# Kernel tuning notes

Measured on AMD Instinct MI355X. Metric: run time of the kernel, lower is better.

## Reference

```python
import jax, jax.numpy as jnp
import numpy as np

OBS = 256      # observation_space_size == state_vector_len
SV = 2047      # STATE_VECTORS = WMG_MAX_OBS
D = 256        # tfm_vec_size = 8 heads * 32 head_size
H = 8
HD = 32
L = 2          # TFM_NUM_LAYERS
FF = 1024      # TFM_HIDDEN_SIZE
ACH = 512      # AC_HIDDEN_LAYER_SIZE
A = 16         # action_space_size


def setup_inputs() -> dict:
    key = jax.random.key(0)
    ks = jax.random.split(key, 24)
    r = lambda k, s: (jax.random.normal(k, s, jnp.float32) * 0.02)
    inp = {
        "observation": jax.random.normal(ks[0], (OBS,), jnp.float32),
        "old_vectors": jax.random.normal(ks[1], (SV, OBS), jnp.float32),
        "W_core": r(ks[2], (OBS, D)), "b_core": jnp.zeros((D,), jnp.float32),
        # memo embedding takes cat(state_vec, age_onehot) of size OBS+SV
        "W_memo": r(ks[3], (OBS + SV, D)), "b_memo": jnp.zeros((D,), jnp.float32),
        "Wq": r(ks[4], (L, D, D)), "bq": jnp.zeros((L, D), jnp.float32),
        "Wk": r(ks[5], (L, D, D)), "bk": jnp.zeros((L, D), jnp.float32),
        "Wv": r(ks[6], (L, D, D)), "bv": jnp.zeros((L, D), jnp.float32),
        "Wo": r(ks[7], (L, D, D)), "bo": jnp.zeros((L, D), jnp.float32),
        "ln1_g": jnp.ones((L, D), jnp.float32), "ln1_b": jnp.zeros((L, D), jnp.float32),
        "ln2_g": jnp.ones((L, D), jnp.float32), "ln2_b": jnp.zeros((L, D), jnp.float32),
        "W_ff1": r(ks[8], (L, D, FF)), "b_ff1": jnp.zeros((L, FF), jnp.float32),
        "W_ff2": r(ks[9], (L, FF, D)), "b_ff2": jnp.zeros((L, D), jnp.float32),
        "aW1": r(ks[10], (D, ACH)), "ab1": jnp.zeros((ACH,), jnp.float32),
        "aW2": r(ks[11], (ACH, ACH)), "ab2": jnp.zeros((ACH,), jnp.float32),
        "aWo": r(ks[12], (ACH, A)), "abo": jnp.zeros((A,), jnp.float32),
        "cW1": r(ks[13], (D, ACH)), "cb1": jnp.zeros((ACH,), jnp.float32),
        "cW2": r(ks[14], (ACH, ACH)), "cb2": jnp.zeros((ACH,), jnp.float32),
        "cWo": r(ks[15], (ACH, 1)), "cbo": jnp.zeros((1,), jnp.float32),
    }
    return inp


def _ln(x, g, b, eps=1e-5):
    m = jnp.mean(x, axis=-1, keepdims=True)
    v = jnp.mean(jnp.square(x - m), axis=-1, keepdims=True)
    return (x - m) * jax.lax.rsqrt(v + eps) * g + b


def reference(observation, old_vectors, W_core, b_core, W_memo, b_memo,
              Wq, bq, Wk, bk, Wv, bv, Wo, bo,
              ln1_g, ln1_b, ln2_g, ln2_b, W_ff1, b_ff1, W_ff2, b_ff2,
              aW1, ab1, aW2, ab2, aWo, abo, cW1, cb1, cW2, cb2, cWo, cbo):
    # core embedding [D]
    emb0 = observation @ W_core + b_core
    # fused memo + age-onehot embedding: cat(vec_i, e_i) @ W_memo == vec_i @ W_memo[:OBS] + W_memo[OBS+i]
    memo_emb = old_vectors @ W_memo[:OBS] + W_memo[OBS:] + b_memo  # [SV, D]
    x = jnp.concatenate([emb0[None, :], memo_emb], axis=0)[None]   # [1, 1+SV, D]
    S = 1 + SV
    scale = 1.0 / np.sqrt(HD).astype(np.float32)
    for l in range(L):
        q = (x @ Wq[l] + bq[l]).reshape(1, S, H, HD)
        k = (x @ Wk[l] + bk[l]).reshape(1, S, H, HD)
        v = (x @ Wv[l] + bv[l]).reshape(1, S, H, HD)
        scores = jnp.einsum('bqhd,bkhd->bhqk', q, k) * scale       # [1,H,S,S]
        probs = jax.nn.softmax(scores, axis=-1)
        ctx = jnp.einsum('bhqk,bkhd->bqhd', probs, v).reshape(1, S, D)
        x = _ln(x + ctx @ Wo[l] + bo[l], ln1_g[l], ln1_b[l])
        h = jax.nn.gelu(x @ W_ff1[l] + b_ff1[l])
        x = _ln(x + h @ W_ff2[l] + b_ff2[l], ln2_g[l], ln2_b[l])
    t = x[:, 0, :]                                                 # [1, D]
    ha = jnp.tanh(jnp.tanh(t @ aW1 + ab1) @ aW2 + ab2)
    policy = ha @ aWo + abo                                        # [1, A] logits
    hc = jnp.tanh(jnp.tanh(t @ cW1 + cb1) @ cW2 + cb2)
    value_est = hc @ cWo + cbo                                     # [1, 1]
    # WMG_MAX_MEMOS == 0 path: new state vector is tanh(observation)
    new_vector = jnp.tanh(observation)                             # [OBS]
    return value_est, policy, new_vector
```

## Files before the change

### kernel.cpp

```cpp
#include <hip/hip_runtime.h>
#include <stdint.h>

typedef __attribute__((ext_vector_type(8))) short bf16x8;
typedef __attribute__((ext_vector_type(4))) float f32x4;

constexpr int kSEQ = 2048;
constexpr int kD   = 256;
constexpr int kHD  = 32;
constexpr int kFF  = 1024;
constexpr int kA   = 16;

__device__ __forceinline__ unsigned short f2b(float f) {
  union { float f; unsigned int u; } v; v.f = f;
  unsigned int r = v.u + 0x7FFFu + ((v.u >> 16) & 1u);
  return (unsigned short)(r >> 16);
}

struct ConvTable {
  const float* src[13];
  int K[13];
  int N[13];
  int dst[13];
  int tstart[14];
};

union SharedU {
  struct { unsigned short lt[64][72]; } cv;
  struct { unsigned short Al[64][40]; unsigned short Bl[32][40]; } g64;
  struct { unsigned short Kl[64][40]; unsigned short Vt[32][72];
           unsigned short Pl[4][16][72]; } at;
  struct { unsigned short As[16][264]; float2 red[4][16]; } lg;
};

struct MegaParams {
  ConvTable tab;
  const float *obs, *oldv, *Wcore, *bcore, *Wmemo0, *bmemo, *Wmemo2;
  const float *bq, *bk, *bv, *bo, *ln1g, *ln1b, *ln2g, *ln2b, *bff1, *bff2;
  const float *aW1, *ab1, *aW2, *ab2, *aWo, *abo;
  const float *cW1, *cb1, *cW2, *cb2, *cWo, *cbo;
  float* xf; unsigned short* xb;
  unsigned short *qb, *kb, *vb, *hb, *wT;
  float *pacc, *pml, *pf, *out;
  int oQKV[2], oWoT[2], oFF1[2], oFF2[2];
  int convJobs, nsplit, tpb;
};

__device__ void conv_job(const MegaParams& p, SharedU& sh, int job) {
  const int tid = threadIdx.x;
  if (job == p.convJobs) {
    float a = p.bcore[tid];
    #pragma unroll 8
    for (int k = 0; k < 256; k++) a += p.obs[k] * p.Wcore[k * kD + tid];
    p.xf[tid] = a;
    p.xb[tid] = f2b(a);
    return;
  }
  int m = 0;
  while (job >= p.tab.tstart[m + 1]) m++;
  const int tloc = job - p.tab.tstart[m];
  const int N = p.tab.N[m], K = p.tab.K[m];
  const int ntile = N >> 6;
  const int k0 = (tloc / ntile) * 64, n0 = (tloc % ntile) * 64;
  const float* src = p.tab.src[m];
  {
    const int r = tid >> 2, c16 = (tid & 3) * 16;
    const float* sp = src + (size_t)(k0 + r) * N + n0 + c16;
    #pragma unroll
    for (int j = 0; j < 16; j++) sh.cv.lt[r][c16 + j] = f2b(sp[j]);
  }
  __syncthreads();
  {
    const int n = tid >> 2, kc = (tid & 3) * 16;
    unsigned short* dp = p.wT + p.tab.dst[m] + (size_t)(n0 + n) * K + k0 + kc;
    unsigned short g[16];
    #pragma unroll
    for (int j = 0; j < 16; j++) g[j] = sh.cv.lt[kc + j][n];
    *(bf16x8*)dp = *(bf16x8*)&g[0];
    *(bf16x8*)(dp + 8) = *(bf16x8*)&g[8];
  }
}

__device__ void memo_job(const MegaParams& p, SharedU& sh, int job) {
  const int tid = threadIdx.x;
  const int w = tid >> 6, l = tid & 63, lg = l >> 4, lr = l & 15;
  const int sr = tid >> 2, sk = (tid & 3) * 8;
  const int kr = tid >> 3, nc = (tid & 7) * 4;
  const int m0 = (job & 31) * 64, n0 = (job >> 5) * 32;
  f32x4 acc[2];
  #pragma unroll
  for (int c = 0; c < 2; c++)
    #pragma unroll
    for (int i = 0; i < 4; i++) acc[c][i] = 0.f;

  auto loadA = [&](int k0) -> bf16x8 {
    bf16x8 av;
    if (m0 + sr < 2047) {
      const float* ap = p.oldv + (size_t)(m0 + sr) * 256 + k0 + sk;
      #pragma unroll
      for (int j = 0; j < 8; j++) av[j] = (short)f2b(ap[j]);
    } else {
      #pragma unroll
      for (int j = 0; j < 8; j++) av[j] = 0;
    }
    return av;
  };
  auto loadB = [&](int k0, float* b4) {
    const float* bp = p.Wmemo0 + (size_t)(k0 + kr) * kD + n0 + nc;
    #pragma unroll
    for (int j = 0; j < 4; j++) b4[j] = bp[j];
  };

  bf16x8 av = loadA(0);
  float b4[4];
  loadB(0, b4);

  for (int k0 = 0; k0 < 256; k0 += 32) {
    __syncthreads();
    *(bf16x8*)&sh.g64.Al[sr][sk] = av;
    #pragma unroll
    for (int j = 0; j < 4; j++) sh.g64.Bl[nc + j][kr] = f2b(b4[j]);
    __syncthreads();
    if (k0 + 32 < 256) {
      av = loadA(k0 + 32);
      loadB(k0 + 32, b4);
    }
    bf16x8 af = *(bf16x8*)&sh.g64.Al[w * 16 + lr][8 * lg];
    #pragma unroll
    for (int c = 0; c < 2; c++) {
      bf16x8 bf = *(bf16x8*)&sh.g64.Bl[c * 16 + lr][8 * lg];
      acc[c] = __builtin_amdgcn_mfma_f32_16x16x32_bf16(af, bf, acc[c], 0, 0, 0);
    }
  }

  #pragma unroll
  for (int c = 0; c < 2; c++)
    #pragma unroll
    for (int i = 0; i < 4; i++) {
      const int gr = m0 + w * 16 + 4 * lg + i;
      const int gc = n0 + c * 16 + lr;
      if (gr >= 2047) continue;
      const float v = acc[c][i] + p.bmemo[gc] + p.Wmemo2[(size_t)gr * kD + gc];
      p.xf[(size_t)(gr + 1) * kD + gc] = v;
      p.xb[(size_t)(gr + 1) * kD + gc] = f2b(v);
    }
}

__global__ __launch_bounds__(256) void k_cvm(MegaParams p) {
  __shared__ SharedU sh;
  if (blockIdx.x < 256) memo_job(p, sh, blockIdx.x);
  else conv_job(p, sh, blockIdx.x - 256);
}

template <int EPI>
__device__ __forceinline__ void gemm_job(
    SharedU& sh, int m0, int n0, const unsigned short* Ap, int lda, int Kloop,
    const unsigned short* BT, int ldb,
    const float* p0, const float* p1, const float* p2,
    void* o0, void* o1, void* o2) {
  const int tid = threadIdx.x;
  const int w = tid >> 6, l = tid & 63, lg = l >> 4, lr = l & 15;
  const int sr = tid >> 2, sk = (tid & 3) * 8;
  f32x4 acc[2];
  #pragma unroll
  for (int c = 0; c < 2; c++)
    #pragma unroll
    for (int i = 0; i < 4; i++) acc[c][i] = 0.f;

  bf16x8 av = *(const bf16x8*)(Ap + (size_t)(m0 + sr) * lda + sk);
  bf16x8 bv;
  if (tid < 128) bv = *(const bf16x8*)(BT + (size_t)(n0 + sr) * ldb + sk);

  for (int k0 = 0; k0 < Kloop; k0 += 32) {
    __syncthreads();
    *(bf16x8*)&sh.g64.Al[sr][sk] = av;
    if (tid < 128) *(bf16x8*)&sh.g64.Bl[sr][sk] = bv;
    __syncthreads();
    if (k0 + 32 < Kloop) {
      av = *(const bf16x8*)(Ap + (size_t)(m0 + sr) * lda + k0 + 32 + sk);
      if (tid < 128)
        bv = *(const bf16x8*)(BT + (size_t)(n0 + sr) * ldb + k0 + 32 + sk);
    }
    bf16x8 af = *(bf16x8*)&sh.g64.Al[w * 16 + lr][8 * lg];
    #pragma unroll
    for (int c = 0; c < 2; c++) {
      bf16x8 bf = *(bf16x8*)&sh.g64.Bl[c * 16 + lr][8 * lg];
      acc[c] = __builtin_amdgcn_mfma_f32_16x16x32_bf16(af, bf, acc[c], 0, 0, 0);
    }
  }

  #pragma unroll
  for (int c = 0; c < 2; c++) {
    #pragma unroll
    for (int i = 0; i < 4; i++) {
      const int gr = m0 + w * 16 + 4 * lg + i;
      const int gc = n0 + c * 16 + lr;
      float v = acc[c][i];
      if constexpr (EPI == 1) {
        const int t = gc >> 8, cc = gc & 255;
        const float* bp = (t == 0) ? p0 : (t == 1 ? p1 : p2);
        unsigned short* op = (t == 0) ? (unsigned short*)o0
                              : (t == 1 ? (unsigned short*)o1
                                        : (unsigned short*)o2);
        v += bp[cc];
        if (t == 0) v *= 0.17677669529663687f;
        op[(size_t)gr * kD + cc] = f2b(v);
      } else if constexpr (EPI == 2) {
        v += p0[gc];
        const float g =
            0.5f * v *
            (1.0f + tanhf(0.7978845608028654f * (v + 0.044715f * v * v * v)));
        ((unsigned short*)o0)[(size_t)gr * kFF + gc] = f2b(g);
      } else {
        ((float*)o0)[(size_t)gr * kD + gc] = v;
      }
    }
  }
}

__global__ __launch_bounds__(256) void k_qkv(MegaParams p, int lyr) {
  __shared__ SharedU sh;
  for (int job = blockIdx.x; job < 768; job += gridDim.x) {
    const int m0 = (job & 31) * 64, n0 = (job >> 5) * 32;
    gemm_job<1>(sh, m0, n0, p.xb, 256, 256, p.wT + p.oQKV[lyr], 256,
                p.bq + lyr * 256, p.bk + lyr * 256, p.bv + lyr * 256,
                p.qb, p.kb, p.vb);
  }
}

__global__ __launch_bounds__(256) void k_ff1(MegaParams p, int lyr) {
  __shared__ SharedU sh;
  for (int job = blockIdx.x; job < 1024; job += gridDim.x) {
    const int m0 = (job & 31) * 64, n0 = (job >> 5) * 32;
    gemm_job<2>(sh, m0, n0, p.xb, 256, 256, p.wT + p.oFF1[lyr], 256,
                p.bff1 + lyr * 1024, nullptr, nullptr, p.hb, nullptr, nullptr);
  }
}

__global__ __launch_bounds__(256) void k_ff2p(MegaParams p, int lyr) {
  __shared__ SharedU sh;
  for (int job = blockIdx.x; job < 1024; job += gridDim.x) {
    const int m0 = (job & 31) * 64;
    const int n0 = ((job >> 5) & 7) * 32;
    const int kc = (job >> 8) * 256;
    gemm_job<3>(sh, m0, n0, p.hb + kc, kFF, 256,
                p.wT + p.oFF2[lyr] + kc, kFF, nullptr, nullptr, nullptr,
                p.pf + (size_t)(job >> 8) * kSEQ * kD, nullptr, nullptr);
  }
}

__device__ void attn_job(SharedU& sh, int qb_, int h, int s, int tpb,
                         const unsigned short* q, const unsigned short* k,
                         const unsigned short* v, float* pacc, float* pml) {
  const int tid = threadIdx.x;
  const int w = tid >> 6, l = tid & 63, lg = l >> 4, lr = l & 15;
  const int q0 = qb_ * 64;
  const int hoff = h * kHD;
  const int sr = tid >> 2, sk = (tid & 3) * 8;
  const int t0 = s * tpb;

  const bf16x8 qf =
      *(const bf16x8*)(q + (size_t)(q0 + w * 16 + lr) * kD + hoff + 8 * lg);

  float m_[4], l_[4];
  f32x4 acc[2];
  #pragma unroll
  for (int i = 0; i < 4; i++) { m_[i] = -1e30f; l_[i] = 0.f; }
  #pragma unroll
  for (int dt = 0; dt < 2; dt++)
    #pragma unroll
    for (int i = 0; i < 4; i++) acc[dt][i] = 0.f;

  bf16x8 kreg = *(const bf16x8*)(k + (size_t)(t0 * 64 + sr) * kD + hoff + sk);
  bf16x8 vreg = *(const bf16x8*)(v + (size_t)(t0 * 64 + sr) * kD + hoff + sk);

  for (int t = 0; t < tpb; t++) {
    __syncthreads();
    *(bf16x8*)&sh.at.Kl[sr][sk] = kreg;
    #pragma unroll
    for (int j = 0; j < 8; j++) sh.at.Vt[sk + j][sr] = (unsigned short)vreg[j];
    __syncthreads();
    if (t + 1 < tpb) {
      const size_t nx = (size_t)((t0 + t + 1) * 64 + sr) * kD + hoff + sk;
      kreg = *(const bf16x8*)(k + nx);
      vreg = *(const bf16x8*)(v + nx);
    }
    f32x4 sc[4];
    #pragma unroll
    for (int c = 0; c < 4; c++) {
      f32x4 z;
      #pragma unroll
      for (int i = 0; i < 4; i++) z[i] = 0.f;
      bf16x8 kf = *(bf16x8*)&sh.at.Kl[c * 16 + lr][8 * lg];
      sc[c] = __builtin_amdgcn_mfma_f32_16x16x32_bf16(qf, kf, z, 0, 0, 0);
    }
    float tm[4];
    #pragma unroll
    for (int i = 0; i < 4; i++)
      tm[i] = fmaxf(fmaxf(sc[0][i], sc[1][i]), fmaxf(sc[2][i], sc[3][i]));
    #pragma unroll
    for (int mm = 1; mm <= 8; mm <<= 1)
      #pragma unroll
      for (int i = 0; i < 4; i++) tm[i] = fmaxf(tm[i], __shfl_xor(tm[i], mm));
    float pv[4][4], rs[4], corr[4];
    #pragma unroll
    for (int i = 0; i < 4; i++) {
      const float nm = fmaxf(m_[i], tm[i]);
      corr[i] = __expf(m_[i] - nm);
      m_[i] = nm;
      rs[i] = 0.f;
    }
    #pragma unroll
    for (int c = 0; c < 4; c++)
      #pragma unroll
      for (int i = 0; i < 4; i++) {
        pv[c][i] = __expf(sc[c][i] - m_[i]);
        rs[i] += pv[c][i];
      }
    #pragma unroll
    for (int mm = 1; mm <= 8; mm <<= 1)
      #pragma unroll
      for (int i = 0; i < 4; i++) rs[i] += __shfl_xor(rs[i], mm);
    #pragma unroll
    for (int i = 0; i < 4; i++) {
      l_[i] = l_[i] * corr[i] + rs[i];
      acc[0][i] *= corr[i];
      acc[1][i] *= corr[i];
    }
    #pragma unroll
    for (int c = 0; c < 4; c++)
      #pragma unroll
      for (int i = 0; i < 4; i++)
        sh.at.Pl[w][4 * lg + i][c * 16 + lr] = f2b(pv[c][i]);
    __syncthreads();
    #pragma unroll
    for (int k2 = 0; k2 < 2; k2++) {
      bf16x8 pf_ = *(bf16x8*)&sh.at.Pl[w][lr][k2 * 32 + 8 * lg];
      #pragma unroll
      for (int dt = 0; dt < 2; dt++) {
        bf16x8 vf = *(bf16x8*)&sh.at.Vt[dt * 16 + lr][k2 * 32 + 8 * lg];
        acc[dt] = __builtin_amdgcn_mfma_f32_16x16x32_bf16(pf_, vf, acc[dt], 0, 0, 0);
      }
    }
  }

  const int pb = s * 8 + h;
  float* pa = pacc + (size_t)pb * kSEQ * kHD;
  float* pm = pml + (size_t)pb * kSEQ * 2;
  #pragma unroll
  for (int dt = 0; dt < 2; dt++)
    #pragma unroll
    for (int i = 0; i < 4; i++) {
      const int gr = q0 + w * 16 + 4 * lg + i;
      pa[(size_t)gr * kHD + dt * 16 + lr] = acc[dt][i];
    }
  if (lr == 0) {
    #pragma unroll
    for (int i = 0; i < 4; i++) {
      const int gr = q0 + w * 16 + 4 * lg + i;
      float2 ml; ml.x = m_[i]; ml.y = l_[i];
      *(float2*)&pm[(size_t)gr * 2] = ml;
    }
  }
}

__global__ __launch_bounds__(256) void k_attn(MegaParams p) {
  __shared__ SharedU sh;
  const int njobs = 256 * p.nsplit;
  for (int job = blockIdx.x; job < njobs; job += gridDim.x) {
    const int qb_ = job & 31, h = (job >> 5) & 7, s = job >> 8;
    attn_job(sh, qb_, h, s, p.tpb, p.qb, p.kb, p.vb, p.pacc, p.pml);
  }
}

__device__ __forceinline__ void ln_write(SharedU& sh, float vloc[4][4], int r0,
                                         const float* gam, const float* bet,
                                         float* xf, unsigned short* xb) {
  const int tid = threadIdx.x;
  const int w = tid >> 6, l = tid & 63, lg = l >> 4, lr = l & 15;
  float ps[4], ps2[4];
  #pragma unroll
  for (int i = 0; i < 4; i++) {
    ps[i] = 0.f; ps2[i] = 0.f;
    #pragma unroll
    for (int c = 0; c < 4; c++) {
      ps[i] += vloc[c][i];
      ps2[i] += vloc[c][i] * vloc[c][i];
    }
  }
  #pragma unroll
  for (int mm = 1; mm <= 8; mm <<= 1)
    #pragma unroll
    for (int i = 0; i < 4; i++) {
      ps[i] += __shfl_xor(ps[i], mm);
      ps2[i] += __shfl_xor(ps2[i], mm);
    }
  if (lr == 0) {
    #pragma unroll
    for (int i = 0; i < 4; i++) {
      float2 t; t.x = ps[i]; t.y = ps2[i];
      sh.lg.red[w][4 * lg + i] = t;
    }
  }
  __syncthreads();
  #pragma unroll
  for (int i = 0; i < 4; i++) {
    const int ri = 4 * lg + i;
    float sx = 0.f, sx2 = 0.f;
    #pragma unroll
    for (int ww = 0; ww < 4; ww++) {
      float2 t = sh.lg.red[ww][ri];
      sx += t.x; sx2 += t.y;
    }
    const float mean = sx * (1.0f / 256.0f);
    const float var = sx2 * (1.0f / 256.0f) - mean * mean;
    const float rstd = rsqrtf(var + 1e-5f);
    const int gr = r0 + ri;
    #pragma unroll
    for (int c = 0; c < 4; c++) {
      const int col = w * 64 + c * 16 + lr;
      const float y = (vloc[c][i] - mean) * rstd * gam[col] + bet[col];
      xf[(size_t)gr * kD + col] = y;
      xb[(size_t)gr * kD + col] = f2b(y);
    }
  }
}

__global__ __launch_bounds__(256) void k_woln(MegaParams p, int lyr) {
  __shared__ SharedU sh;
  const unsigned short* BT = p.wT + p.oWoT[lyr];
  const float* bias = p.bo + lyr * kD;
  const float* gam = p.ln1g + lyr * kD;
  const float* bet = p.ln1b + lyr * kD;
  const int tid = threadIdx.x;
  const int w = tid >> 6, l = tid & 63, lg = l >> 4, lr = l & 15;
  for (int job = blockIdx.x; job < 128; job += gridDim.x) {
    const int r0 = job * 16;
    __syncthreads();
    {
      const int row = r0 + (tid >> 4);
      const int kc = (tid & 15) * 16;
      const int h_ = kc >> 5;
      float mx = -1e30f;
      for (int s2 = 0; s2 < p.nsplit; s2++)
        mx = fmaxf(mx, p.pml[((size_t)(s2 * 8 + h_) * kSEQ + row) * 2]);
      float L = 0.f;
      const int d0 = kc & 31;
      float o[16];
      #pragma unroll
      for (int j = 0; j < 16; j++) o[j] = 0.f;
      for (int s2 = 0; s2 < p.nsplit; s2++) {
        const size_t pb = (size_t)(s2 * 8 + h_) * kSEQ + row;
        const float2 t = *(const float2*)&p.pml[pb * 2];
        const float es = __expf(t.x - mx);
        L += t.y * es;
        const float* pa = p.pacc + pb * kHD + d0;
        #pragma unroll
        for (int j = 0; j < 16; j++) o[j] += pa[j] * es;
      }
      const float inv = 1.0f / L;
      unsigned short* dst = &sh.lg.As[tid >> 4][kc];
      #pragma unroll
      for (int j = 0; j < 16; j++) dst[j] = f2b(o[j] * inv);
    }
    __syncthreads();
    f32x4 acc[4];
    #pragma unroll
    for (int c = 0; c < 4; c++)
      #pragma unroll
      for (int i = 0; i < 4; i++) acc[c][i] = 0.f;
    #pragma unroll 2
    for (int k0 = 0; k0 < 256; k0 += 32) {
      bf16x8 af = *(bf16x8*)&sh.lg.As[lr][k0 + 8 * lg];
      #pragma unroll
      for (int c = 0; c < 4; c++) {
        bf16x8 bf = *(const bf16x8*)(BT + (size_t)(w * 64 + c * 16 + lr) * 256 +
                                     k0 + 8 * lg);
        acc[c] = __builtin_amdgcn_mfma_f32_16x16x32_bf16(af, bf, acc[c], 0, 0, 0);
      }
    }
    float vloc[4][4];
    #pragma unroll
    for (int c = 0; c < 4; c++)
      #pragma unroll
      for (int i = 0; i < 4; i++) {
        const int col = w * 64 + c * 16 + lr;
        const int gr = r0 + 4 * lg + i;
        vloc[c][i] = acc[c][i] + bias[col] + p.xf[(size_t)gr * kD + col];
      }
    ln_write(sh, vloc, r0, gam, bet, p.xf, p.xb);
  }
}

template <bool WH>
__global__ __launch_bounds__(256) void k_ln2r(MegaParams p, int lyr) {
  __shared__ float tl[256];
  __shared__ float hA[1024];
  __shared__ float hB[1024];
  __shared__ float vred[4];
  const float* bias = p.bff2 + lyr * kD;
  const float* gam = p.ln2g + lyr * kD;
  const float* bet = p.ln2b + lyr * kD;
  const int tid = threadIdx.x;
  const int w = tid >> 6, l = tid & 63;
  const int row = blockIdx.x * 4 + w;
  f32x4 v = *(const f32x4*)(p.xf + (size_t)row * kD + l * 4);
  f32x4 b4 = *(const f32x4*)(bias + l * 4);
  #pragma unroll
  for (int i = 0; i < 4; i++) v[i] += b4[i];
  #pragma unroll
  for (int s = 0; s < 4; s++) {
    f32x4 t = *(const f32x4*)(p.pf + ((size_t)s * kSEQ + row) * kD + l * 4);
    #pragma unroll
    for (int i = 0; i < 4; i++) v[i] += t[i];
  }
  float su = v[0] + v[1] + v[2] + v[3];
  #pragma unroll
  for (int mm = 1; mm < 64; mm <<= 1) su += __shfl_xor(su, mm);
  const float mn = su * (1.0f / 256.0f);
  const float d0 = v[0] - mn, d1 = v[1] - mn, d2 = v[2] - mn, d3 = v[3] - mn;
  float s2 = d0 * d0 + d1 * d1 + d2 * d2 + d3 * d3;
  #pragma unroll
  for (int mm = 1; mm < 64; mm <<= 1) s2 += __shfl_xor(s2, mm);
  const float rstd = rsqrtf(s2 * (1.0f / 256.0f) + 1e-5f);
  f32x4 g4 = *(const f32x4*)(gam + l * 4);
  f32x4 be4 = *(const f32x4*)(bet + l * 4);
  f32x4 y;
  y[0] = d0 * rstd * g4[0] + be4[0];
  y[1] = d1 * rstd * g4[1] + be4[1];
  y[2] = d2 * rstd * g4[2] + be4[2];
  y[3] = d3 * rstd * g4[3] + be4[3];
  *(f32x4*)(p.xf + (size_t)row * kD + l * 4) = y;
  unsigned long long pk = (unsigned long long)f2b(y[0]) |
                          ((unsigned long long)f2b(y[1]) << 16) |
                          ((unsigned long long)f2b(y[2]) << 32) |
                          ((unsigned long long)f2b(y[3]) << 48);
  *(unsigned long long*)(p.xb + (size_t)row * kD + l * 4) = pk;

  if constexpr (WH) {
    if (blockIdx.x == 0) {
      if (w == 0) *(f32x4*)&tl[l * 4] = y;
      __syncthreads();
      float a0 = p.ab1[tid], a1 = p.ab1[tid + 256];
      float c0 = p.cb1[tid], c1 = p.cb1[tid + 256];
      for (int k = 0; k < 256; k++) {
        const float x = tl[k];
        a0 += x * p.aW1[(size_t)k * 512 + tid];
        a1 += x * p.aW1[(size_t)k * 512 + tid + 256];
        c0 += x * p.cW1[(size_t)k * 512 + tid];
        c1 += x * p.cW1[(size_t)k * 512 + tid + 256];
      }
      hA[tid] = tanhf(a0); hA[tid + 256] = tanhf(a1);
      hA[512 + tid] = tanhf(c0); hA[768 + tid] = tanhf(c1);
      __syncthreads();
      float b0 = p.ab2[tid], b1 = p.ab2[tid + 256];
      float e0 = p.cb2[tid], e1 = p.cb2[tid + 256];
      for (int k = 0; k < 512; k++) {
        const float xa = hA[k], xc = hA[512 + k];
        b0 += xa * p.aW2[(size_t)k * 512 + tid];
        b1 += xa * p.aW2[(size_t)k * 512 + tid + 256];
        e0 += xc * p.cW2[(size_t)k * 512 + tid];
        e1 += xc * p.cW2[(size_t)k * 512 + tid + 256];
      }
      hB[tid] = tanhf(b0); hB[tid + 256] = tanhf(b1);
      hB[512 + tid] = tanhf(e0); hB[768 + tid] = tanhf(e1);
      __syncthreads();
      const int g = tid >> 4, l16 = tid & 15;
      float s = 0.f;
      for (int k2 = l16 * 32; k2 < l16 * 32 + 32; k2++)
        s += hB[k2] * p.aWo[(size_t)k2 * kA + g];
      #pragma unroll
      for (int mm = 1; mm <= 8; mm <<= 1) s += __shfl_xor(s, mm);
      if (l16 == 0) p.out[1 + g] = s + p.abo[g];
      float vv = hB[512 + tid] * p.cWo[tid] + hB[768 + tid] * p.cWo[tid + 256];
      #pragma unroll
      for (int mm = 1; mm <= 32; mm <<= 1) vv += __shfl_xor(vv, mm);
      if ((tid & 63) == 0) vred[tid >> 6] = vv;
      __syncthreads();
      if (tid == 0)
        p.out[0] = vred[0] + vred[1] + vred[2] + vred[3] + p.cbo[0];
      p.out[17 + tid] = tanhf(p.obs[tid]);
    }
  }
}

extern "C" void kernel_launch(void* const* d_in, const int* in_sizes, int n_in,
                              void* d_out, int out_size, void* d_ws, size_t ws_size,
                              hipStream_t stream) {
  const float* obs   = (const float*)d_in[0];
  const float* oldv  = (const float*)d_in[1];
  const float* Wcore = (const float*)d_in[2];
  const float* bcore = (const float*)d_in[3];
  const float* Wmemo = (const float*)d_in[4];
  const float* bmemo = (const float*)d_in[5];
  const float* Wq    = (const float*)d_in[6];
  const float* bq    = (const float*)d_in[7];
  const float* Wk    = (const float*)d_in[8];
  const float* bk    = (const float*)d_in[9];
  const float* Wv    = (const float*)d_in[10];
  const float* bv    = (const float*)d_in[11];
  const float* Wo    = (const float*)d_in[12];
  const float* bo    = (const float*)d_in[13];
  const float* ln1g  = (const float*)d_in[14];
  const float* ln1b  = (const float*)d_in[15];
  const float* ln2g  = (const float*)d_in[16];
  const float* ln2b  = (const float*)d_in[17];
  const float* Wff1  = (const float*)d_in[18];
  const float* bff1  = (const float*)d_in[19];
  const float* Wff2  = (const float*)d_in[20];
  const float* bff2  = (const float*)d_in[21];

  MegaParams P;
  P.obs = obs; P.oldv = oldv; P.Wcore = Wcore; P.bcore = bcore;
  P.Wmemo0 = Wmemo; P.bmemo = bmemo; P.Wmemo2 = Wmemo + 256 * 256;
  P.bq = bq; P.bk = bk; P.bv = bv; P.bo = bo;
  P.ln1g = ln1g; P.ln1b = ln1b; P.ln2g = ln2g; P.ln2b = ln2b;
  P.bff1 = bff1; P.bff2 = bff2;
  P.aW1 = (const float*)d_in[22]; P.ab1 = (const float*)d_in[23];
  P.aW2 = (const float*)d_in[24]; P.ab2 = (const float*)d_in[25];
  P.aWo = (const float*)d_in[26]; P.abo = (const float*)d_in[27];
  P.cW1 = (const float*)d_in[28]; P.cb1 = (const float*)d_in[29];
  P.cW2 = (const float*)d_in[30]; P.cb2 = (const float*)d_in[31];
  P.cWo = (const float*)d_in[32]; P.cbo = (const float*)d_in[33];

  char* ws = (char*)d_ws;
  P.xf = (float*)(ws + 0);
  P.xb = (unsigned short*)(ws + (2u << 20));
  P.qb = (unsigned short*)(ws + (3u << 20));
  P.kb = (unsigned short*)(ws + (4u << 20));
  P.vb = (unsigned short*)(ws + (5u << 20));
  P.hb = (unsigned short*)(ws + (6u << 20));
  P.wT = (unsigned short*)(ws + (10u << 20));
  P.out = (float*)d_out;

  int nsplit = 8;
  const size_t paccOff = (size_t)14u << 20;
  const size_t pmlOff  = (size_t)31u << 20;
  const size_t pfOff   = (size_t)33u << 20;
  while (nsplit > 1 &&
         (paccOff + (size_t)nsplit * 8 * kSEQ * kHD * 4 > pmlOff ||
          pfOff + (size_t)4 * kSEQ * kD * 4 > ws_size))
    nsplit >>= 1;
  P.pacc = (float*)(ws + paccOff);
  P.pml  = (float*)(ws + pmlOff);
  P.pf   = (float*)(ws + pfOff);
  P.nsplit = nsplit;
  P.tpb = 32 / nsplit;

  int cur = 0;
  for (int l2 = 0; l2 < 2; l2++) {
    P.oQKV[l2] = cur; cur += 196608;
    P.oWoT[l2] = cur; cur += 65536;
    P.oFF1[l2] = cur; cur += 262144;
    P.oFF2[l2] = cur; cur += 262144;
  }

  int idx = 0, ts = 0;
  auto add = [&](const float* s, int K, int N, int dst) {
    P.tab.src[idx] = s; P.tab.K[idx] = K; P.tab.N[idx] = N;
    P.tab.dst[idx] = dst; P.tab.tstart[idx] = ts;
    ts += (K >> 6) * (N >> 6); idx++;
  };
  for (int l2 = 0; l2 < 2; l2++) {
    add(Wq + l2 * 65536, 256, 256, P.oQKV[l2]);
    add(Wk + l2 * 65536, 256, 256, P.oQKV[l2] + 65536);
    add(Wv + l2 * 65536, 256, 256, P.oQKV[l2] + 131072);
    add(Wo + l2 * 65536, 256, 256, P.oWoT[l2]);
    add(Wff1 + l2 * 262144, 256, 1024, P.oFF1[l2]);
    add(Wff2 + l2 * 262144, 1024, 256, P.oFF2[l2]);
  }
  P.tab.tstart[idx] = ts;
  P.convJobs = ts;

  k_cvm<<<256 + ts + 1, 256, 0, stream>>>(P);
  for (int lyr = 0; lyr < 2; lyr++) {
    k_qkv<<<768, 256, 0, stream>>>(P, lyr);
    k_attn<<<256 * nsplit, 256, 0, stream>>>(P);
    k_woln<<<128, 256, 0, stream>>>(P, lyr);
    k_ff1<<<1024, 256, 0, stream>>>(P, lyr);
    k_ff2p<<<1024, 256, 0, stream>>>(P, lyr);
    if (lyr == 0) k_ln2r<false><<<512, 256, 0, stream>>>(P, lyr);
    else          k_ln2r<true><<<512, 256, 0, stream>>>(P, lyr);
  }
}
```

Baseline: 236.5 us.

## Fuse Wo+LN1+FFN+LN2+next-layer QKV into one row-block kernel and parallelise head MLP

Replaces the separate Wo/LN1, FF1, split-K FF2, and LN2 kernels with one kernel per 16-row block. It keeps the LN1 output and the GELU hidden activations in shared memory, and for layer 0 also computes layer 1's QKV projection. The actor/critic head, previously run serially in a single block, is split across three small multi-block kernels. This removes the hidden-activation and split-K partial round-trips through global memory and several launches. In exchange, only 128 blocks do the large FFN work, each streaming the full weight matrices with low MFMA tile reuse.

```diff
diff --git a/kernel.cpp b/kernel.cpp
--- a/kernel.cpp
+++ b/kernel.cpp
@@ -29,7 +29,6 @@
   struct { unsigned short Al[64][40]; unsigned short Bl[32][40]; } g64;
   struct { unsigned short Kl[64][40]; unsigned short Vt[32][72];
            unsigned short Pl[4][16][72]; } at;
-  struct { unsigned short As[16][264]; float2 red[4][16]; } lg;
 };
 
 struct MegaParams {
@@ -39,8 +38,8 @@
   const float *aW1, *ab1, *aW2, *ab2, *aWo, *abo;
   const float *cW1, *cb1, *cW2, *cb2, *cWo, *cbo;
   float* xf; unsigned short* xb;
-  unsigned short *qb, *kb, *vb, *hb, *wT;
-  float *pacc, *pml, *pf, *out;
+  unsigned short *qb, *kb, *vb, *wT;
+  float *pacc, *pml, *h1, *h2, *out;
   int oQKV[2], oWoT[2], oFF1[2], oFF2[2];
   int convJobs, nsplit, tpb;
 };
@@ -151,34 +150,33 @@
   else conv_job(p, sh, blockIdx.x - 256);
 }
 
-template <int EPI>
-__device__ __forceinline__ void gemm_job(
-    SharedU& sh, int m0, int n0, const unsigned short* Ap, int lda, int Kloop,
-    const unsigned short* BT, int ldb,
-    const float* p0, const float* p1, const float* p2,
-    void* o0, void* o1, void* o2) {
+__global__ __launch_bounds__(256) void k_qkv(MegaParams p, int lyr) {
+  __shared__ SharedU sh;
   const int tid = threadIdx.x;
   const int w = tid >> 6, l = tid & 63, lg = l >> 4, lr = l & 15;
   const int sr = tid >> 2, sk = (tid & 3) * 8;
+  const int job = blockIdx.x;
+  const int m0 = (job & 31) * 64, n0 = (job >> 5) * 32;
+  const unsigned short* BT = p.wT + p.oQKV[lyr];
   f32x4 acc[2];
   #pragma unroll
   for (int c = 0; c < 2; c++)
     #pragma unroll
     for (int i = 0; i < 4; i++) acc[c][i] = 0.f;
 
-  bf16x8 av = *(const bf16x8*)(Ap + (size_t)(m0 + sr) * lda + sk);
+  bf16x8 av = *(const bf16x8*)(p.xb + (size_t)(m0 + sr) * 256 + sk);
   bf16x8 bv;
-  if (tid < 128) bv = *(const bf16x8*)(BT + (size_t)(n0 + sr) * ldb + sk);
-
-  for (int k0 = 0; k0 < Kloop; k0 += 32) {
+  if (tid < 128) bv = *(const bf16x8*)(BT + (size_t)(n0 + sr) * 256 + sk);
+
+  for (int k0 = 0; k0 < 256; k0 += 32) {
     __syncthreads();
     *(bf16x8*)&sh.g64.Al[sr][sk] = av;
     if (tid < 128) *(bf16x8*)&sh.g64.Bl[sr][sk] = bv;
     __syncthreads();
-    if (k0 + 32 < Kloop) {
-      av = *(const bf16x8*)(Ap + (size_t)(m0 + sr) * lda + k0 + 32 + sk);
+    if (k0 + 32 < 256) {
+      av = *(const bf16x8*)(p.xb + (size_t)(m0 + sr) * 256 + k0 + 32 + sk);
       if (tid < 128)
-        bv = *(const bf16x8*)(BT + (size_t)(n0 + sr) * ldb + k0 + 32 + sk);
+        bv = *(const bf16x8*)(BT + (size_t)(n0 + sr) * 256 + k0 + 32 + sk);
     }
     bf16x8 af = *(bf16x8*)&sh.g64.Al[w * 16 + lr][8 * lg];
     #pragma unroll
@@ -189,63 +187,19 @@
   }
 
   #pragma unroll
-  for (int c = 0; c < 2; c++) {
+  for (int c = 0; c < 2; c++)
     #pragma unroll
     for (int i = 0; i < 4; i++) {
       const int gr = m0 + w * 16 + 4 * lg + i;
       const int gc = n0 + c * 16 + lr;
-      float v = acc[c][i];
-      if constexpr (EPI == 1) {
-        const int t = gc >> 8, cc = gc & 255;
-        const float* bp = (t == 0) ? p0 : (t == 1 ? p1 : p2);
-        unsigned short* op = (t == 0) ? (unsigned short*)o0
-                              : (t == 1 ? (unsigned short*)o1
-                                        : (unsigned short*)o2);
-        v += bp[cc];
-        if (t == 0) v *= 0.17677669529663687f;
-        op[(size_t)gr * kD + cc] = f2b(v);
-      } else if constexpr (EPI == 2) {
-        v += p0[gc];
-        const float g =
-            0.5f * v *
-            (1.0f + tanhf(0.7978845608028654f * (v + 0.044715f * v * v * v)));
-        ((unsigned short*)o0)[(size_t)gr * kFF + gc] = f2b(g);
-      } else {
-        ((float*)o0)[(size_t)gr * kD + gc] = v;
-      }
-    }
-  }
-}
-
-__global__ __launch_bounds__(256) void k_qkv(MegaParams p, int lyr) {
-  __shared__ SharedU sh;
-  for (int job = blockIdx.x; job < 768; job += gridDim.x) {
-    const int m0 = (job & 31) * 64, n0 = (job >> 5) * 32;
-    gemm_job<1>(sh, m0, n0, p.xb, 256, 256, p.wT + p.oQKV[lyr], 256,
-                p.bq + lyr * 256, p.bk + lyr * 256, p.bv + lyr * 256,
-                p.qb, p.kb, p.vb);
-  }
-}
-
-__global__ __launch_bounds__(256) void k_ff1(MegaParams p, int lyr) {
-  __shared__ SharedU sh;
-  for (int job = blockIdx.x; job < 1024; job += gridDim.x) {
-    const int m0 = (job & 31) * 64, n0 = (job >> 5) * 32;
-    gemm_job<2>(sh, m0, n0, p.xb, 256, 256, p.wT + p.oFF1[lyr], 256,
-                p.bff1 + lyr * 1024, nullptr, nullptr, p.hb, nullptr, nullptr);
-  }
-}
-
-__global__ __launch_bounds__(256) void k_ff2p(MegaParams p, int lyr) {
-  __shared__ SharedU sh;
-  for (int job = blockIdx.x; job < 1024; job += gridDim.x) {
-    const int m0 = (job & 31) * 64;
-    const int n0 = ((job >> 5) & 7) * 32;
-    const int kc = (job >> 8) * 256;
-    gemm_job<3>(sh, m0, n0, p.hb + kc, kFF, 256,
-                p.wT + p.oFF2[lyr] + kc, kFF, nullptr, nullptr, nullptr,
-                p.pf + (size_t)(job >> 8) * kSEQ * kD, nullptr, nullptr);
-  }
+      const int t = gc >> 8, cc = gc & 255;
+      const float* bp = (t == 0) ? (p.bq + lyr * 256)
+                        : (t == 1 ? (p.bk + lyr * 256) : (p.bv + lyr * 256));
+      unsigned short* op = (t == 0) ? p.qb : (t == 1 ? p.kb : p.vb);
+      float v = acc[c][i] + bp[cc];
+      if (t == 0) v *= 0.17677669529663687f;
+      op[(size_t)gr * kD + cc] = f2b(v);
+    }
 }
 
 __device__ void attn_job(SharedU& sh, int qb_, int h, int s, int tpb,
@@ -365,26 +319,22 @@
 
 __global__ __launch_bounds__(256) void k_attn(MegaParams p) {
   __shared__ SharedU sh;
-  const int njobs = 256 * p.nsplit;
-  for (int job = blockIdx.x; job < njobs; job += gridDim.x) {
-    const int qb_ = job & 31, h = (job >> 5) & 7, s = job >> 8;
-    attn_job(sh, qb_, h, s, p.tpb, p.qb, p.kb, p.vb, p.pacc, p.pml);
-  }
-}
-
-__device__ __forceinline__ void ln_write(SharedU& sh, float vloc[4][4], int r0,
-                                         const float* gam, const float* bet,
-                                         float* xf, unsigned short* xb) {
-  const int tid = threadIdx.x;
-  const int w = tid >> 6, l = tid & 63, lg = l >> 4, lr = l & 15;
+  const int job = blockIdx.x;
+  const int qb_ = job & 31, h = (job >> 5) & 7, s = job >> 8;
+  attn_job(sh, qb_, h, s, p.tpb, p.qb, p.kb, p.vb, p.pacc, p.pml);
+}
+
+__device__ __forceinline__ void ln16(float v[4][4], float2 (*red)[16],
+                                     const float* gam, const float* bet,
+                                     int w, int lg, int lr) {
   float ps[4], ps2[4];
   #pragma unroll
   for (int i = 0; i < 4; i++) {
     ps[i] = 0.f; ps2[i] = 0.f;
     #pragma unroll
     for (int c = 0; c < 4; c++) {
-      ps[i] += vloc[c][i];
-      ps2[i] += vloc[c][i] * vloc[c][i];
+      ps[i] += v[c][i];
+      ps2[i] += v[c][i] * v[c][i];
     }
   }
   #pragma unroll
@@ -398,7 +348,7 @@
     #pragma unroll
     for (int i = 0; i < 4; i++) {
       float2 t; t.x = ps[i]; t.y = ps2[i];
-      sh.lg.red[w][4 * lg + i] = t;
+      red[w][4 * lg + i] = t;
     }
   }
   __syncthreads();
@@ -408,61 +358,61 @@
     float sx = 0.f, sx2 = 0.f;
     #pragma unroll
     for (int ww = 0; ww < 4; ww++) {
-      float2 t = sh.lg.red[ww][ri];
+      float2 t = red[ww][ri];
       sx += t.x; sx2 += t.y;
     }
     const float mean = sx * (1.0f / 256.0f);
     const float var = sx2 * (1.0f / 256.0f) - mean * mean;
     const float rstd = rsqrtf(var + 1e-5f);
-    const int gr = r0 + ri;
     #pragma unroll
     for (int c = 0; c < 4; c++) {
       const int col = w * 64 + c * 16 + lr;
-      const float y = (vloc[c][i] - mean) * rstd * gam[col] + bet[col];
-      xf[(size_t)gr * kD + col] = y;
-      xb[(size_t)gr * kD + col] = f2b(y);
-    }
-  }
-}
-
-__global__ __launch_bounds__(256) void k_woln(MegaParams p, int lyr) {
-  __shared__ SharedU sh;
-  const unsigned short* BT = p.wT + p.oWoT[lyr];
-  const float* bias = p.bo + lyr * kD;
-  const float* gam = p.ln1g + lyr * kD;
-  const float* bet = p.ln1b + lyr * kD;
+      v[c][i] = (v[c][i] - mean) * rstd * gam[col] + bet[col];
+    }
+  }
+}
+
+template <bool QKV>
+__global__ __launch_bounds__(256) void k_block(MegaParams p, int lyr) {
+  __shared__ unsigned short As[16][264];
+  __shared__ unsigned short Hs[16][1032];
+  __shared__ float2 red[4][16];
   const int tid = threadIdx.x;
   const int w = tid >> 6, l = tid & 63, lg = l >> 4, lr = l & 15;
-  for (int job = blockIdx.x; job < 128; job += gridDim.x) {
-    const int r0 = job * 16;
-    __syncthreads();
-    {
-      const int row = r0 + (tid >> 4);
-      const int kc = (tid & 15) * 16;
-      const int h_ = kc >> 5;
-      float mx = -1e30f;
-      for (int s2 = 0; s2 < p.nsplit; s2++)
-        mx = fmaxf(mx, p.pml[((size_t)(s2 * 8 + h_) * kSEQ + row) * 2]);
-      float L = 0.f;
-      const int d0 = kc & 31;
-      float o[16];
-      #pragma unroll
-      for (int j = 0; j < 16; j++) o[j] = 0.f;
-      for (int s2 = 0; s2 < p.nsplit; s2++) {
-        const size_t pb = (size_t)(s2 * 8 + h_) * kSEQ + row;
-        const float2 t = *(const float2*)&p.pml[pb * 2];
-        const float es = __expf(t.x - mx);
-        L += t.y * es;
-        const float* pa = p.pacc + pb * kHD + d0;
-        #pragma unroll
-        for (int j = 0; j < 16; j++) o[j] += pa[j] * es;
-      }
-      const float inv = 1.0f / L;
-      unsigned short* dst = &sh.lg.As[tid >> 4][kc];
-      #pragma unroll
-      for (int j = 0; j < 16; j++) dst[j] = f2b(o[j] * inv);
-    }
-    __syncthreads();
+  const int r0 = blockIdx.x * 16;
+
+  {
+    const int row = r0 + (tid >> 4);
+    const int kc = (tid & 15) * 16;
+    const int h_ = kc >> 5;
+    const int d0 = kc & 31;
+    float mx = -1e30f;
+    for (int s2 = 0; s2 < p.nsplit; s2++)
+      mx = fmaxf(mx, p.pml[((size_t)(s2 * 8 + h_) * kSEQ + row) * 2]);
+    float L = 0.f;
+    float o[16];
+    #pragma unroll
+    for (int j = 0; j < 16; j++) o[j] = 0.f;
+    for (int s2 = 0; s2 < p.nsplit; s2++) {
+      const size_t pb = (size_t)(s2 * 8 + h_) * kSEQ + row;
+      const float2 t = *(const float2*)&p.pml[pb * 2];
+      const float es = __expf(t.x - mx);
+      L += t.y * es;
+      const float* pa = p.pacc + pb * kHD + d0;
+      #pragma unroll
+      for (int j = 0; j < 16; j++) o[j] += pa[j] * es;
+    }
+    const float inv = 1.0f / L;
+    unsigned short* dst = &As[tid >> 4][kc];
+    #pragma unroll
+    for (int j = 0; j < 16; j++) dst[j] = f2b(o[j] * inv);
+  }
+  __syncthreads();
+
+  float yv[4][4];
+  {
+    const unsigned short* BT = p.wT + p.oWoT[lyr];
+    const float* bias = p.bo + lyr * kD;
     f32x4 acc[4];
     #pragma unroll
     for (int c = 0; c < 4; c++)
@@ -470,7 +420,7 @@
       for (int i = 0; i < 4; i++) acc[c][i] = 0.f;
     #pragma unroll 2
     for (int k0 = 0; k0 < 256; k0 += 32) {
-      bf16x8 af = *(bf16x8*)&sh.lg.As[lr][k0 + 8 * lg];
+      bf16x8 af = *(bf16x8*)&As[lr][k0 + 8 * lg];
       #pragma unroll
       for (int c = 0; c < 4; c++) {
         bf16x8 bf = *(const bf16x8*)(BT + (size_t)(w * 64 + c * 16 + lr) * 256 +
@@ -478,109 +428,196 @@
         acc[c] = __builtin_amdgcn_mfma_f32_16x16x32_bf16(af, bf, acc[c], 0, 0, 0);
       }
     }
-    float vloc[4][4];
     #pragma unroll
     for (int c = 0; c < 4; c++)
       #pragma unroll
       for (int i = 0; i < 4; i++) {
         const int col = w * 64 + c * 16 + lr;
         const int gr = r0 + 4 * lg + i;
-        vloc[c][i] = acc[c][i] + bias[col] + p.xf[(size_t)gr * kD + col];
-      }
-    ln_write(sh, vloc, r0, gam, bet, p.xf, p.xb);
-  }
-}
-
-template <bool WH>
-__global__ __launch_bounds__(256) void k_ln2r(MegaParams p, int lyr) {
+        yv[c][i] = acc[c][i] + bias[col] + p.xf[(size_t)gr * kD + col];
+      }
+    ln16(yv, red, p.ln1g + lyr * kD, p.ln1b + lyr * kD, w, lg, lr);
+    #pragma unroll
+    for (int c = 0; c < 4; c++)
+      #pragma unroll
+      for (int i = 0; i < 4; i++)
+        As[4 * lg + i][w * 64 + c * 16 + lr] = f2b(yv[c][i]);
+  }
+  __syncthreads();
+
+  {
+    const unsigned short* BT = p.wT + p.oFF1[lyr];
+    const float* bias = p.bff1 + lyr * kFF;
+    #pragma unroll 2
+    for (int ct = 0; ct < 16; ct++) {
+      f32x4 acc;
+      #pragma unroll
+      for (int i = 0; i < 4; i++) acc[i] = 0.f;
+      #pragma unroll
+      for (int k0 = 0; k0 < 256; k0 += 32) {
+        bf16x8 af = *(bf16x8*)&As[lr][k0 + 8 * lg];
+        bf16x8 bf = *(const bf16x8*)(
+            BT + (size_t)(w * 256 + ct * 16 + lr) * 256 + k0 + 8 * lg);
+        acc = __builtin_amdgcn_mfma_f32_16x16x32_bf16(af, bf, acc, 0, 0, 0);
+      }
+      const int col = w * 256 + ct * 16 + lr;
+      #pragma unroll
+      for (int i = 0; i < 4; i++) {
+        const float v = acc[i] + bias[col];
+        const float g =
+            0.5f * v *
+            (1.0f + tanhf(0.7978845608028654f * (v + 0.044715f * v * v * v)));
+        Hs[4 * lg + i][col] = f2b(g);
+      }
+    }
+  }
+  __syncthreads();
+
+  float zv[4][4];
+  {
+    const unsigned short* BT = p.wT + p.oFF2[lyr];
+    const float* bias = p.bff2 + lyr * kD;
+    f32x4 acc[4];
+    #pragma unroll
+    for (int c = 0; c < 4; c++)
+      #pragma unroll
+      for (int i = 0; i < 4; i++) acc[c][i] = 0.f;
+    #pragma unroll 2
+    for (int k0 = 0; k0 < 1024; k0 += 32) {
+      bf16x8 af = *(bf16x8*)&Hs[lr][k0 + 8 * lg];
+      #pragma unroll
+      for (int c = 0; c < 4; c++) {
+        bf16x8 bf = *(const bf16x8*)(
+            BT + (size_t)(w * 64 + c * 16 + lr) * 1024 + k0 + 8 * lg);
+        acc[c] = __builtin_amdgcn_mfma_f32_16x16x32_bf16(af, bf, acc[c], 0, 0, 0);
+      }
+    }
+    #pragma unroll
+    for (int c = 0; c < 4; c++)
+      #pragma unroll
+      for (int i = 0; i < 4; i++) {
+        const int col = w * 64 + c * 16 + lr;
+        zv[c][i] = acc[c][i] + bias[col] + yv[c][i];
+      }
+    ln16(zv, red, p.ln2g + lyr * kD, p.ln2b + lyr * kD, w, lg, lr);
+    #pragma unroll
+    for (int c = 0; c < 4; c++)
+      #pragma unroll
+      for (int i = 0; i < 4; i++) {
+        const int col = w * 64 + c * 16 + lr;
+        const int gr = r0 + 4 * lg + i;
+        p.xf[(size_t)gr * kD + col] = zv[c][i];
+        p.xb[(size_t)gr * kD + col] = f2b(zv[c][i]);
+        if constexpr (QKV) As[4 * lg + i][col] = f2b(zv[c][i]);
+      }
+  }
+
+  if constexpr (QKV) {
+    __syncthreads();
+    const unsigned short* BT = p.wT + p.oQKV[lyr + 1];
+    const float* bq_ = p.bq + (lyr + 1) * 256;
+    const float* bk_ = p.bk + (lyr + 1) * 256;
+    const float* bv_ = p.bv + (lyr + 1) * 256;
+    #pragma unroll 2
+    for (int t = 0; t < 12; t++) {
+      f32x4 acc;
+      #pragma unroll
+      for (int i = 0; i < 4; i++) acc[i] = 0.f;
+      #pragma unroll
+      for (int k0 = 0; k0 < 256; k0 += 32) {
+        bf16x8 af = *(bf16x8*)&As[lr][k0 + 8 * lg];
+        bf16x8 bf = *(const bf16x8*)(
+            BT + (size_t)(w * 192 + t * 16 + lr) * 256 + k0 + 8 * lg);
+        acc = __builtin_amdgcn_mfma_f32_16x16x32_bf16(af, bf, acc, 0, 0, 0);
+      }
+      const int gc = w * 192 + t * 16 + lr;
+      const int tb = gc >> 8, cc = gc & 255;
+      const float* bp = (tb == 0) ? bq_ : (tb == 1 ? bk_ : bv_);
+      unsigned short* op = (tb == 0) ? p.qb : (tb == 1 ? p.kb : p.vb);
+      #pragma unroll
+      for (int i = 0; i < 4; i++) {
+        const int gr = r0 + 4 * lg + i;
+        float v = acc[i] + bp[cc];
+        if (tb == 0) v *= 0.17677669529663687f;
+        op[(size_t)gr * kD + cc] = f2b(v);
+      }
+    }
+  }
+}
+
+__global__ __launch_bounds__(256) void k_h1(MegaParams p) {
   __shared__ float tl[256];
-  __shared__ float hA[1024];
-  __shared__ float hB[1024];
-  __shared__ float vred[4];
-  const float* bias = p.bff2 + lyr * kD;
-  const float* gam = p.ln2g + lyr * kD;
-  const float* bet = p.ln2b + lyr * kD;
+  __shared__ float red[4][64];
   const int tid = threadIdx.x;
-  const int w = tid >> 6, l = tid & 63;
-  const int row = blockIdx.x * 4 + w;
-  f32x4 v = *(const f32x4*)(p.xf + (size_t)row * kD + l * 4);
-  f32x4 b4 = *(const f32x4*)(bias + l * 4);
-  #pragma unroll
-  for (int i = 0; i < 4; i++) v[i] += b4[i];
-  #pragma unroll
-  for (int s = 0; s < 4; s++) {
-    f32x4 t = *(const f32x4*)(p.pf + ((size_t)s * kSEQ + row) * kD + l * 4);
-    #pragma unroll
-    for (int i = 0; i < 4; i++) v[i] += t[i];
-  }
-  float su = v[0] + v[1] + v[2] + v[3];
-  #pragma unroll
-  for (int mm = 1; mm < 64; mm <<= 1) su += __shfl_xor(su, mm);
-  const float mn = su * (1.0f / 256.0f);
-  const float d0 = v[0] - mn, d1 = v[1] - mn, d2 = v[2] - mn, d3 = v[3] - mn;
-  float s2 = d0 * d0 + d1 * d1 + d2 * d2 + d3 * d3;
-  #pragma unroll
-  for (int mm = 1; mm < 64; mm <<= 1) s2 += __shfl_xor(s2, mm);
-  const float rstd = rsqrtf(s2 * (1.0f / 256.0f) + 1e-5f);
-  f32x4 g4 = *(const f32x4*)(gam + l * 4);
-  f32x4 be4 = *(const f32x4*)(bet + l * 4);
-  f32x4 y;
-  y[0] = d0 * rstd * g4[0] + be4[0];
-  y[1] = d1 * rstd * g4[1] + be4[1];
-  y[2] = d2 * rstd * g4[2] + be4[2];
-  y[3] = d3 * rstd * g4[3] + be4[3];
-  *(f32x4*)(p.xf + (size_t)row * kD + l * 4) = y;
-  unsigned long long pk = (unsigned long long)f2b(y[0]) |
-                          ((unsigned long long)f2b(y[1]) << 16) |
-                          ((unsigned long long)f2b(y[2]) << 32) |
-                          ((unsigned long long)f2b(y[3]) << 48);
-  *(unsigned long long*)(p.xb + (size_t)row * kD + l * 4) = pk;
-
-  if constexpr (WH) {
-    if (blockIdx.x == 0) {
-      if (w == 0) *(f32x4*)&tl[l * 4] = y;
-      __syncthreads();
-      float a0 = p.ab1[tid], a1 = p.ab1[tid + 256];
-      float c0 = p.cb1[tid], c1 = p.cb1[tid + 256];
-      for (int k = 0; k < 256; k++) {
-        const float x = tl[k];
-        a0 += x * p.aW1[(size_t)k * 512 + tid];
-        a1 += x * p.aW1[(size_t)k * 512 + tid + 256];
-        c0 += x * p.cW1[(size_t)k * 512 + tid];
-        c1 += x * p.cW1[(size_t)k * 512 + tid + 256];
-      }
-      hA[tid] = tanhf(a0); hA[tid + 256] = tanhf(a1);
-      hA[512 + tid] = tanhf(c0); hA[768 + tid] = tanhf(c1);
-      __syncthreads();
-      float b0 = p.ab2[tid], b1 = p.ab2[tid + 256];
-      float e0 = p.cb2[tid], e1 = p.cb2[tid + 256];
-      for (int k = 0; k < 512; k++) {
-        const float xa = hA[k], xc = hA[512 + k];
-        b0 += xa * p.aW2[(size_t)k * 512 + tid];
-        b1 += xa * p.aW2[(size_t)k * 512 + tid + 256];
-        e0 += xc * p.cW2[(size_t)k * 512 + tid];
-        e1 += xc * p.cW2[(size_t)k * 512 + tid + 256];
-      }
-      hB[tid] = tanhf(b0); hB[tid + 256] = tanhf(b1);
-      hB[512 + tid] = tanhf(e0); hB[768 + tid] = tanhf(e1);
-      __syncthreads();
-      const int g = tid >> 4, l16 = tid & 15;
-      float s = 0.f;
-      for (int k2 = l16 * 32; k2 < l16 * 32 + 32; k2++)
-        s += hB[k2] * p.aWo[(size_t)k2 * kA + g];
-      #pragma unroll
-      for (int mm = 1; mm <= 8; mm <<= 1) s += __shfl_xor(s, mm);
-      if (l16 == 0) p.out[1 + g] = s + p.abo[g];
-      float vv = hB[512 + tid] * p.cWo[tid] + hB[768 + tid] * p.cWo[tid + 256];
-      #pragma unroll
-      for (int mm = 1; mm <= 32; mm <<= 1) vv += __shfl_xor(vv, mm);
-      if ((tid & 63) == 0) vred[tid >> 6] = vv;
-      __syncthreads();
-      if (tid == 0)
-        p.out[0] = vred[0] + vred[1] + vred[2] + vred[3] + p.cbo[0];
-      p.out[17 + tid] = tanhf(p.obs[tid]);
-    }
-  }
+  tl[tid] = p.xf[tid];
+  __syncthreads();
+  const int jj = blockIdx.x * 64;
+  const bool actor = jj < 512;
+  const float* W = actor ? p.aW1 : p.cW1;
+  const float* b = actor ? p.ab1 : p.cb1;
+  const int j0 = actor ? jj : jj - 512;
+  const int ks = tid >> 6, j = tid & 63;
+  float s = 0.f;
+  #pragma unroll 4
+  for (int k2 = ks * 64; k2 < ks * 64 + 64; k2++)
+    s += tl[k2] * W[(size_t)k2 * 512 + j0 + j];
+  red[ks][j] = s;
+  __syncthreads();
+  if (tid < 64) {
+    float t = red[0][tid] + red[1][tid] + red[2][tid] + red[3][tid] + b[j0 + tid];
+    p.h1[jj + tid] = tanhf(t);
+  }
+}
+
+__global__ __launch_bounds__(256) void k_h2(MegaParams p) {
+  __shared__ float tl[512];
+  __shared__ float red[4][64];
+  const int tid = threadIdx.x;
+  const int jj = blockIdx.x * 64;
+  const bool actor = jj < 512;
+  const float* hin = actor ? p.h1 : p.h1 + 512;
+  tl[tid] = hin[tid];
+  tl[tid + 256] = hin[tid + 256];
+  __syncthreads();
+  const float* W = actor ? p.aW2 : p.cW2;
+  const float* b = actor ? p.ab2 : p.cb2;
+  const int j0 = actor ? jj : jj - 512;
+  const int ks = tid >> 6, j = tid & 63;
+  float s = 0.f;
+  #pragma unroll 4
+  for (int k2 = ks * 128; k2 < ks * 128 + 128; k2++)
+    s += tl[k2] * W[(size_t)k2 * 512 + j0 + j];
+  red[ks][j] = s;
+  __syncthreads();
+  if (tid < 64) {
+    float t = red[0][tid] + red[1][tid] + red[2][tid] + red[3][tid] + b[j0 + tid];
+    p.h2[jj + tid] = tanhf(t);
+  }
+}
+
+__global__ __launch_bounds__(256) void k_h3(MegaParams p) {
+  __shared__ float ha[512], hc[512], vred[4];
+  const int tid = threadIdx.x;
+  ha[tid] = p.h2[tid];
+  ha[tid + 256] = p.h2[tid + 256];
+  hc[tid] = p.h2[512 + tid];
+  hc[tid + 256] = p.h2[768 + tid];
+  __syncthreads();
+  const int g = tid >> 4, l16 = tid & 15;
+  float s = 0.f;
+  for (int k2 = l16 * 32; k2 < l16 * 32 + 32; k2++)
+    s += ha[k2] * p.aWo[(size_t)k2 * kA + g];
+  #pragma unroll
+  for (int mm = 1; mm <= 8; mm <<= 1) s += __shfl_xor(s, mm);
+  if (l16 == 0) p.out[1 + g] = s + p.abo[g];
+  float vv = hc[tid] * p.cWo[tid] + hc[tid + 256] * p.cWo[tid + 256];
+  #pragma unroll
+  for (int mm = 1; mm <= 32; mm <<= 1) vv += __shfl_xor(vv, mm);
+  if ((tid & 63) == 0) vred[tid >> 6] = vv;
+  __syncthreads();
+  if (tid == 0)
+    p.out[0] = vred[0] + vred[1] + vred[2] + vred[3] + p.cbo[0];
+  p.out[17 + tid] = tanhf(p.obs[tid]);
 }
 
 extern "C" void kernel_launch(void* const* d_in, const int* in_sizes, int n_in,
@@ -628,21 +665,20 @@
   P.qb = (unsigned short*)(ws + (3u << 20));
   P.kb = (unsigned short*)(ws + (4u << 20));
   P.vb = (unsigned short*)(ws + (5u << 20));
-  P.hb = (unsigned short*)(ws + (6u << 20));
-  P.wT = (unsigned short*)(ws + (10u << 20));
+  P.wT = (unsigned short*)(ws + (6u << 20));
+  P.h1 = (float*)(ws + (10u << 20));
+  P.h2 = (float*)(ws + (10u << 20) + 8192);
   P.out = (float*)d_out;
 
   int nsplit = 8;
   const size_t paccOff = (size_t)14u << 20;
   const size_t pmlOff  = (size_t)31u << 20;
-  const size_t pfOff   = (size_t)33u << 20;
   while (nsplit > 1 &&
          (paccOff + (size_t)nsplit * 8 * kSEQ * kHD * 4 > pmlOff ||
-          pfOff + (size_t)4 * kSEQ * kD * 4 > ws_size))
+          pmlOff + (size_t)nsplit * 8 * kSEQ * 2 * 4 > ws_size))
     nsplit >>= 1;
   P.pacc = (float*)(ws + paccOff);
   P.pml  = (float*)(ws + pmlOff);
-  P.pf   = (float*)(ws + pfOff);
   P.nsplit = nsplit;
   P.tpb = 32 / nsplit;
 
@@ -672,13 +708,12 @@
   P.convJobs = ts;
 
   k_cvm<<<256 + ts + 1, 256, 0, stream>>>(P);
-  for (int lyr = 0; lyr < 2; lyr++) {
-    k_qkv<<<768, 256, 0, stream>>>(P, lyr);
-    k_attn<<<256 * nsplit, 256, 0, stream>>>(P);
-    k_woln<<<128, 256, 0, stream>>>(P, lyr);
-    k_ff1<<<1024, 256, 0, stream>>>(P, lyr);
-    k_ff2p<<<1024, 256, 0, stream>>>(P, lyr);
-    if (lyr == 0) k_ln2r<false><<<512, 256, 0, stream>>>(P, lyr);
-    else          k_ln2r<true><<<512, 256, 0, stream>>>(P, lyr);
-  }
-}
+  k_qkv<<<768, 256, 0, stream>>>(P, 0);
+  k_attn<<<256 * nsplit, 256, 0, stream>>>(P);
+  k_block<true><<<128, 256, 0, stream>>>(P, 0);
+  k_attn<<<256 * nsplit, 256, 0, stream>>>(P);
+  k_block<false><<<128, 256, 0, stream>>>(P, 1);
+  k_h1<<<16, 256, 0, stream>>>(P);
+  k_h2<<<16, 256, 0, stream>>>(P);
+  k_h3<<<1, 256, 0, stream>>>(P);
+}
```

Result: faster. 217.3 us (-8.1%).
